# Kernel tuning notes

Hardware: AMD Instinct MI355X
Metric: run time of the kernel (lower is better)

## Reference

```python
import jax, jax.numpy as jnp
import numpy as np
from jax.scipy.stats import norm as jnorm

BLOCK_SIZE = 64
NUM_BITS = 4
OFFSET = 0.9677083


def make_symmetric_nf_table(num_bits=NUM_BITS, offset=OFFSET):
    # create_normal_map(symmetric=True): midpoints of ppf grid, normalized by max
    variations = 2 ** num_bits
    p = jnp.linspace(1.0 - offset, offset, variations + 1)
    v = jnorm.ppf(p)
    vals = 0.5 * (v[:-1] + v[1:])  # [variations]
    vals = jnp.sort(vals)
    return (vals / vals.max()).astype(jnp.float32)


def setup_inputs() -> dict:
    key = jax.random.key(0)
    k1, k2 = jax.random.split(key)
    M, N = 4096, 4096
    T = 8192  # tokens
    x = jax.random.normal(k1, (T, N), dtype=jnp.float32)
    weight = jax.random.normal(k2, (M, N), dtype=jnp.float32) * 0.02
    # init_max_val: per-block abs max of the flattened weight
    wb = weight.reshape(-1, BLOCK_SIZE)
    max_val = jnp.max(jnp.abs(wb), axis=-1)  # [M*N/block_size]
    lookup_table = make_symmetric_nf_table()  # [16]
    return {"x": x, "weight": weight, "max_val": max_val, "lookup_table": lookup_table}


def reference(x, weight, max_val, lookup_table):
    M, N = weight.shape
    # blockwise quantize: [num_blocks, block_size]
    wb = weight.reshape(-1, BLOCK_SIZE)
    wdiv = wb / max_val[:, None]
    # nearest codebook level: [num_blocks, block_size, num_levels] abs-diff argmin
    idx = jnp.argmin(jnp.abs(wdiv[..., None] - lookup_table[None, None, :]), axis=-1)
    qweight = (lookup_table[idx] * max_val[:, None]).reshape(M, N)
    y = x @ qweight.T  # [T, M]
    return (y, qweight)
```

## Files before the change

### kernel.cpp

```cpp
#include <hip/hip_runtime.h>
#include <stdint.h>
#include <stddef.h>

typedef __attribute__((ext_vector_type(8))) short short8;
typedef __attribute__((ext_vector_type(4))) float f32x4;
typedef __attribute__((ext_vector_type(4))) int i32x4;

#define T_DIM 8192
#define M_DIM 4096
#define K_DIM 4096

__device__ __forceinline__ unsigned short f2b(float f) {
    unsigned int u = __builtin_bit_cast(unsigned int, f);
    u += 0x7fffu + ((u >> 16) & 1u);
    return (unsigned short)(u >> 16);
}

__device__ __forceinline__ void async_copy16(const void* g, const void* l) {
    __builtin_amdgcn_global_load_lds(
        (const __attribute__((address_space(1))) unsigned int*)g,
        (__attribute__((address_space(3))) unsigned int*)l,
        16, 0, 0);
}

__global__ __launch_bounds__(512) void prep_all(const float* __restrict__ w,
                                                const float* __restrict__ maxval,
                                                const float* __restrict__ lut_g,
                                                float* __restrict__ qw,
                                                signed char* __restrict__ wq,
                                                float* __restrict__ cw,
                                                const float* __restrict__ x,
                                                signed char* __restrict__ xq,
                                                float* __restrict__ sx) {
    __shared__ float wm[8];
    __shared__ float lut[16];
    const int tid = threadIdx.x;

    if (blockIdx.x < 4096) {
        const int m = blockIdx.x;
        if (tid < 16) lut[tid] = lut_g[tid];

        size_t base = ((size_t)m * 512 + tid) * 8;
        float mv = maxval[base >> 6];

        float mx = mv;
        #pragma unroll
        for (int off = 1; off < 64; off <<= 1)
            mx = fmaxf(mx, __shfl_xor(mx, off, 64));
        if ((tid & 63) == 0) wm[tid >> 6] = mx;
        __syncthreads();
        float cwm = fmaxf(fmaxf(fmaxf(wm[0], wm[1]), fmaxf(wm[2], wm[3])),
                          fmaxf(fmaxf(wm[4], wm[5]), fmaxf(wm[6], wm[7])));

        float4 w0 = *reinterpret_cast<const float4*>(w + base);
        float4 w1 = *reinterpret_cast<const float4*>(w + base + 4);
        float vin[8] = {w0.x, w0.y, w0.z, w0.w, w1.x, w1.y, w1.z, w1.w};
        float outv[8];
        int   li[8];

        #pragma unroll
        for (int e = 0; e < 8; ++e) {
            float v = vin[e] / mv;
            float bd = fabsf(v - lut[0]);
            int best = 0;
            #pragma unroll
            for (int k = 1; k < 16; ++k) {
                float d = fabsf(v - lut[k]);
                if (d < bd) { bd = d; best = k; }
            }
            outv[e] = lut[best] * mv;
            li[e]   = best;
        }

        float4 o0; o0.x = outv[0]; o0.y = outv[1]; o0.z = outv[2]; o0.w = outv[3];
        float4 o1; o1.x = outv[4]; o1.y = outv[5]; o1.z = outv[6]; o1.w = outv[7];
        *reinterpret_cast<float4*>(qw + base)     = o0;
        *reinterpret_cast<float4*>(qw + base + 4) = o1;

        if (wq != nullptr) {
            float s = 127.0f * mv / cwm;
            unsigned u0 = 0, u1 = 0;
            #pragma unroll
            for (int e = 0; e < 4; ++e) {
                int q = (int)rintf(lut[li[e]] * s);
                u0 |= ((unsigned)(q & 255)) << (8 * e);
            }
            #pragma unroll
            for (int e = 0; e < 4; ++e) {
                int q = (int)rintf(lut[li[4 + e]] * s);
                u1 |= ((unsigned)(q & 255)) << (8 * e);
            }
            uint2 pk; pk.x = u0; pk.y = u1;
            *reinterpret_cast<uint2*>(wq + base) = pk;
            if (tid == 0) cw[m] = cwm;
        }
    } else {
        if (xq == nullptr) return;
        const int row = blockIdx.x - 4096;
        const float* xr = x + (size_t)row * K_DIM;

        float4 a = *reinterpret_cast<const float4*>(xr + tid * 8);
        float4 b = *reinterpret_cast<const float4*>(xr + tid * 8 + 4);
        float v[8] = {a.x, a.y, a.z, a.w, b.x, b.y, b.z, b.w};

        float mx = 0.0f;
        #pragma unroll
        for (int e = 0; e < 8; ++e) mx = fmaxf(mx, fabsf(v[e]));
        #pragma unroll
        for (int off = 1; off < 64; off <<= 1)
            mx = fmaxf(mx, __shfl_xor(mx, off, 64));
        if ((tid & 63) == 0) wm[tid >> 6] = mx;
        __syncthreads();
        float rmax = fmaxf(fmaxf(fmaxf(wm[0], wm[1]), fmaxf(wm[2], wm[3])),
                           fmaxf(fmaxf(wm[4], wm[5]), fmaxf(wm[6], wm[7])));
        float inv = rmax > 0.0f ? 127.0f / rmax : 0.0f;

        unsigned u0 = 0, u1 = 0;
        #pragma unroll
        for (int e = 0; e < 4; ++e) {
            int q = (int)rintf(v[e] * inv);
            q = q > 127 ? 127 : (q < -127 ? -127 : q);
            u0 |= ((unsigned)(q & 255)) << (8 * e);
        }
        #pragma unroll
        for (int e = 0; e < 4; ++e) {
            int q = (int)rintf(v[4 + e] * inv);
            q = q > 127 ? 127 : (q < -127 ? -127 : q);
            u1 |= ((unsigned)(q & 255)) << (8 * e);
        }
        uint2 pk; pk.x = u0; pk.y = u1;
        *reinterpret_cast<uint2*>(xq + (size_t)row * K_DIM + tid * 8) = pk;

        if (tid == 0) sx[row] = rmax / 16129.0f;
    }
}


#define RD_A8(BUF, MH)                                                        \
  { _Pragma("unroll") for (int mi = 0; mi < 4; ++mi) {                        \
        int r_ = wr * 64 + mi * 16 + fr;                                      \
        aI[mi] = *reinterpret_cast<const i32x4*>(                             \
            lds + (BUF) * 32768 + (MH) * 16384 + r_ * 64 +                    \
            (fkB ^ (((r_ >> 1) & 3) << 4)));                                  \
  } }

#define RD_B8(BUF, NH, DST)                                                   \
  { _Pragma("unroll") for (int ni = 0; ni < 2; ++ni) {                        \
        int r_ = wc * 32 + ni * 16 + fr;                                      \
        DST[ni] = *reinterpret_cast<const i32x4*>(                            \
            lds + (BUF) * 32768 + ((NH) ? 8192 : 24576) + r_ * 64 +           \
            (fkB ^ (((r_ >> 1) & 3) << 4)));                                  \
  } }

#define MFMA_Q(MH, NH, B)                                                     \
    _Pragma("unroll") for (int mi = 0; mi < 4; ++mi)                          \
    _Pragma("unroll") for (int ni = 0; ni < 2; ++ni)                          \
        acci[(MH) * 4 + mi][(NH) * 2 + ni] =                                  \
            __builtin_amdgcn_mfma_i32_16x16x64_i8(                            \
                aI[mi], B[ni],                                                \
                acci[(MH) * 4 + mi][(NH) * 2 + ni], 0, 0, 0);

#define PH_A(BUF, TNXT)                                                       \
  { RD_A8(BUF, 0)                                                             \
    RD_B8(BUF, 0, bI0)                                                        \
    RD_B8(BUF, 1, bI1)                                                        \
    stage_r2(TNXT);                                                           \
    asm volatile("" ::: "memory");                                            \
    __builtin_amdgcn_s_barrier();                                             \
    asm volatile("" ::: "memory");                                            \
    __builtin_amdgcn_s_setprio(1);                                            \
    MFMA_Q(0, 0, bI0)                                                         \
    MFMA_Q(0, 1, bI1)                                                         \
    __builtin_amdgcn_s_setprio(0); }

#define PH_B(BUF, TNXT2)                                                      \
  { RD_A8(BUF, 1)                                                             \
    stage_r013(TNXT2);                                                        \
    asm volatile("s_waitcnt vmcnt(3)" ::: "memory");                          \
    __builtin_amdgcn_s_barrier();                                             \
    asm volatile("" ::: "memory");                                            \
    __builtin_amdgcn_s_setprio(1);                                            \
    MFMA_Q(1, 1, bI1)                                                         \
    MFMA_Q(1, 0, bI0)                                                         \
    __builtin_amdgcn_s_setprio(0); }

__global__ __launch_bounds__(512, 2) void gemm_i8(
    const signed char* __restrict__ Aq,
    const signed char* __restrict__ Bq,
    const float* __restrict__ sxp,
    const float* __restrict__ cwp,
    float* __restrict__ Y) {
    __shared__ __align__(16) unsigned char lds[65536];

    const int tid  = threadIdx.x;
    const int lane = tid & 63;
    const int wid  = tid >> 6;
    const int wr   = wid >> 2;
    const int wc   = wid & 3;

    const int bid  = blockIdx.x;
    const int swz  = (bid & 7) * 64 + (bid >> 3);
    const int brow = swz >> 4;
    const int bcol = swz & 15;
    const int row0 = brow * 256;
    const int col0 = bcol * 256;

    const int fr  = lane & 15;
    const int fkB = (lane >> 4) * 16;

    i32x4 acci[8][4] = {};
    i32x4 aI[4], bI0[2], bI1[2];

    const int srow  = wid * 16 + (lane >> 2);
    const int sslot = ((lane & 3) ^ ((srow >> 1) & 3)) * 16;
    const unsigned sdst = wid * 1024u;

    auto stage_r013 = [&](int t) {
        int tc  = t < 64 ? t : 63;
        unsigned boff = (unsigned)(t & 1) * 32768u;
        {
            const char* g = (const char*)Aq +
                (size_t)(row0 + ((srow >> 6) << 7) + (srow & 63)) * K_DIM + tc * 64 + sslot;
            async_copy16(g, lds + boff + sdst); }
        {
            const char* g = (const char*)Bq +
                (size_t)(col0 + ((srow >> 5) << 6) + 32 + (srow & 31)) * K_DIM + tc * 64 + sslot;
            async_copy16(g, lds + boff + 8192u + sdst); }
        {
            const char* g = (const char*)Bq +
                (size_t)(col0 + ((srow >> 5) << 6) + (srow & 31)) * K_DIM + tc * 64 + sslot;
            async_copy16(g, lds + boff + 24576u + sdst); }
    };
    auto stage_r2 = [&](int t) {
        int tc  = t < 64 ? t : 63;
        unsigned boff = (unsigned)(t & 1) * 32768u;
        const char* g = (const char*)Aq +
            (size_t)(row0 + 64 + ((srow >> 6) << 7) + (srow & 63)) * K_DIM + tc * 64 + sslot;
        async_copy16(g, lds + boff + 16384u + sdst);
    };

    stage_r013(0);
    stage_r2(0);
    stage_r013(1);
    asm volatile("s_waitcnt vmcnt(3)" ::: "memory");
    __builtin_amdgcn_s_barrier();
    asm volatile("" ::: "memory");

    for (int i = 0; i < 32; ++i) {
        PH_A(0, 2 * i + 1)
        PH_B(0, 2 * i + 2)
        PH_A(1, 2 * i + 2)
        PH_B(1, 2 * i + 3)
    }
    asm volatile("s_waitcnt vmcnt(0)" ::: "memory");

    const int rb = (lane >> 4) * 4;
    float cwv[4];
    #pragma unroll
    for (int n = 0; n < 4; ++n) cwv[n] = cwp[col0 + wc * 64 + n * 16 + fr];
    #pragma unroll
    for (int m = 0; m < 8; ++m) {
        const int t0 = row0 + wr * 128 + m * 16 + rb;
        f32x4 sx4 = *reinterpret_cast<const f32x4*>(sxp + t0);
        #pragma unroll
        for (int n = 0; n < 4; ++n)
            #pragma unroll
            for (int r = 0; r < 4; ++r)
                Y[(size_t)(t0 + r) * M_DIM + col0 + wc * 64 + n * 16 + fr] =
                    (float)acci[m][n][r] * sx4[r] * cwv[n];
    }
}

__global__ __launch_bounds__(256) void gemm_fb(const float* __restrict__ Ap,
                                               const float* __restrict__ Bp,
                                               float* __restrict__ Y) {
    constexpr int BK = 64;
    __shared__ unsigned short lA[128 * BK];
    __shared__ unsigned short lB[128 * BK];

    const int tid  = threadIdx.x;
    const int lane = tid & 63;
    const int wid  = tid >> 6;
    const int wr   = wid >> 1;
    const int wc   = wid & 1;
    const int brow = blockIdx.x >> 5;
    const int bcol = blockIdx.x & 31;
    const int row0 = brow * 128;
    const int col0 = bcol * 128;

    f32x4 acc[4][4] = {};
    const int fr = lane & 15;
    const int fk = (lane >> 4) * 8;
    const int srow = lane >> 3;
    const int scol = (lane & 7) * 8;

    for (int k0 = 0; k0 < K_DIM; k0 += BK) {
        #pragma unroll
        for (int i = 0; i < 4; ++i) {
            const int c = wid * 4 + i;
            const int r = c * 8 + srow;
            const float* g = Ap + (size_t)(row0 + r) * K_DIM + k0 + scol;
            float4 v0 = *reinterpret_cast<const float4*>(g);
            float4 v1 = *reinterpret_cast<const float4*>(g + 4);
            short8 pk;
            pk[0] = (short)f2b(v0.x); pk[1] = (short)f2b(v0.y);
            pk[2] = (short)f2b(v0.z); pk[3] = (short)f2b(v0.w);
            pk[4] = (short)f2b(v1.x); pk[5] = (short)f2b(v1.y);
            pk[6] = (short)f2b(v1.z); pk[7] = (short)f2b(v1.w);
            *reinterpret_cast<short8*>(lA + c * 512 + lane * 8) = pk;
        }
        #pragma unroll
        for (int i = 0; i < 4; ++i) {
            const int c = wid * 4 + i;
            const int r = c * 8 + srow;
            const float* g = Bp + (size_t)(col0 + r) * K_DIM + k0 + scol;
            float4 v0 = *reinterpret_cast<const float4*>(g);
            float4 v1 = *reinterpret_cast<const float4*>(g + 4);
            short8 pk;
            pk[0] = (short)f2b(v0.x); pk[1] = (short)f2b(v0.y);
            pk[2] = (short)f2b(v0.z); pk[3] = (short)f2b(v0.w);
            pk[4] = (short)f2b(v1.x); pk[5] = (short)f2b(v1.y);
            pk[6] = (short)f2b(v1.z); pk[7] = (short)f2b(v1.w);
            *reinterpret_cast<short8*>(lB + c * 512 + lane * 8) = pk;
        }
        __syncthreads();
        #pragma unroll
        for (int kk = 0; kk < BK; kk += 32) {
            short8 af[4], bfr[4];
            #pragma unroll
            for (int m = 0; m < 4; ++m)
                af[m] = *reinterpret_cast<const short8*>(
                    lA + (wr * 64 + m * 16 + fr) * BK + kk + fk);
            #pragma unroll
            for (int n = 0; n < 4; ++n)
                bfr[n] = *reinterpret_cast<const short8*>(
                    lB + (wc * 64 + n * 16 + fr) * BK + kk + fk);
            #pragma unroll
            for (int m = 0; m < 4; ++m)
                #pragma unroll
                for (int n = 0; n < 4; ++n)
                    acc[m][n] = __builtin_amdgcn_mfma_f32_16x16x32_bf16(
                        af[m], bfr[n], acc[m][n], 0, 0, 0);
        }
        __syncthreads();
    }

    const int orow  = row0 + wr * 64;
    const int ocol  = col0 + wc * 64 + fr;
    const int rbase = (lane >> 4) * 4;
    #pragma unroll
    for (int m = 0; m < 4; ++m)
        #pragma unroll
        for (int n = 0; n < 4; ++n)
            #pragma unroll
            for (int r = 0; r < 4; ++r)
                Y[(size_t)(orow + m * 16 + rbase + r) * M_DIM + ocol + n * 16] =
                    acc[m][n][r];
}

extern "C" void kernel_launch(void* const* d_in, const int* in_sizes, int n_in,
                              void* d_out, int out_size, void* d_ws, size_t ws_size,
                              hipStream_t stream) {
    const float* x   = (const float*)d_in[0];
    const float* w   = (const float*)d_in[1];
    const float* mv  = (const float*)d_in[2];
    const float* lut = (const float*)d_in[3];

    float* y  = (float*)d_out;
    float* qw = y + (size_t)T_DIM * M_DIM;

    const bool full = ws_size >= (49u << 20);

    signed char* xq  = (signed char*)d_ws;
    signed char* wqp = xq + (32u << 20);
    float*       sx  = (float*)(xq + (48u << 20));
    float*       cw  = (float*)(xq + (48u << 20) + 65536);

    if (full) {
        prep_all<<<dim3(12288), dim3(512), 0, stream>>>(
            w, mv, lut, qw, wqp, cw, x, xq, sx);
        gemm_i8<<<dim3(512), dim3(512), 0, stream>>>(xq, wqp, sx, cw, y);
    } else {
        prep_all<<<dim3(4096), dim3(512), 0, stream>>>(
            w, mv, lut, qw, nullptr, nullptr, x, nullptr, nullptr);
        dim3 grid((T_DIM / 128) * (M_DIM / 128));
        gemm_fb<<<grid, dim3(256), 0, stream>>>(x, qw, y);
    }
}
```

Baseline: 208.1 us.

## Switch int8 GEMM to triple-buffered LDS with one barrier per k-step

```diff
diff --git a/kernel.cpp b/kernel.cpp
--- a/kernel.cpp
+++ b/kernel.cpp
@@ -136,53 +136,29 @@
 }
 
 
-#define RD_A8(BUF, MH)                                                        \
+#define RD_A8(BOFS, MH, DST)                                                  \
   { _Pragma("unroll") for (int mi = 0; mi < 4; ++mi) {                        \
         int r_ = wr * 64 + mi * 16 + fr;                                      \
-        aI[mi] = *reinterpret_cast<const i32x4*>(                             \
-            lds + (BUF) * 32768 + (MH) * 16384 + r_ * 64 +                    \
+        DST[mi] = *reinterpret_cast<const i32x4*>(                            \
+            lds + (BOFS) + (MH) * 16384 + r_ * 64 +                           \
             (fkB ^ (((r_ >> 1) & 3) << 4)));                                  \
   } }
 
-#define RD_B8(BUF, NH, DST)                                                   \
+#define RD_B8(BOFS, NH, DST)                                                  \
   { _Pragma("unroll") for (int ni = 0; ni < 2; ++ni) {                        \
         int r_ = wc * 32 + ni * 16 + fr;                                      \
         DST[ni] = *reinterpret_cast<const i32x4*>(                            \
-            lds + (BUF) * 32768 + ((NH) ? 8192 : 24576) + r_ * 64 +           \
+            lds + (BOFS) + ((NH) ? 8192 : 24576) + r_ * 64 +                  \
             (fkB ^ (((r_ >> 1) & 3) << 4)));                                  \
   } }
 
-#define MFMA_Q(MH, NH, B)                                                     \
+#define MFMA_Q(MH, NH, A, B)                                                  \
     _Pragma("unroll") for (int mi = 0; mi < 4; ++mi)                          \
     _Pragma("unroll") for (int ni = 0; ni < 2; ++ni)                          \
         acci[(MH) * 4 + mi][(NH) * 2 + ni] =                                  \
             __builtin_amdgcn_mfma_i32_16x16x64_i8(                            \
-                aI[mi], B[ni],                                                \
+                A[mi], B[ni],                                                 \
                 acci[(MH) * 4 + mi][(NH) * 2 + ni], 0, 0, 0);
-
-#define PH_A(BUF, TNXT)                                                       \
-  { RD_A8(BUF, 0)                                                             \
-    RD_B8(BUF, 0, bI0)                                                        \
-    RD_B8(BUF, 1, bI1)                                                        \
-    stage_r2(TNXT);                                                           \
-    asm volatile("" ::: "memory");                                            \
-    __builtin_amdgcn_s_barrier();                                             \
-    asm volatile("" ::: "memory");                                            \
-    __builtin_amdgcn_s_setprio(1);                                            \
-    MFMA_Q(0, 0, bI0)                                                         \
-    MFMA_Q(0, 1, bI1)                                                         \
-    __builtin_amdgcn_s_setprio(0); }
-
-#define PH_B(BUF, TNXT2)                                                      \
-  { RD_A8(BUF, 1)                                                             \
-    stage_r013(TNXT2);                                                        \
-    asm volatile("s_waitcnt vmcnt(3)" ::: "memory");                          \
-    __builtin_amdgcn_s_barrier();                                             \
-    asm volatile("" ::: "memory");                                            \
-    __builtin_amdgcn_s_setprio(1);                                            \
-    MFMA_Q(1, 1, bI1)                                                         \
-    MFMA_Q(1, 0, bI0)                                                         \
-    __builtin_amdgcn_s_setprio(0); }
 
 __global__ __launch_bounds__(512, 2) void gemm_i8(
     const signed char* __restrict__ Aq,
@@ -190,7 +166,7 @@
     const float* __restrict__ sxp,
     const float* __restrict__ cwp,
     float* __restrict__ Y) {
-    __shared__ __align__(16) unsigned char lds[65536];
+    __shared__ __align__(16) unsigned char lds[98304];
 
     const int tid  = threadIdx.x;
     const int lane = tid & 63;
@@ -209,48 +185,56 @@
     const int fkB = (lane >> 4) * 16;
 
     i32x4 acci[8][4] = {};
-    i32x4 aI[4], bI0[2], bI1[2];
+    i32x4 aI0[4], aI1[4], bI0[2], bI1[2];
 
     const int srow  = wid * 16 + (lane >> 2);
     const int sslot = ((lane & 3) ^ ((srow >> 1) & 3)) * 16;
     const unsigned sdst = wid * 1024u;
 
-    auto stage_r013 = [&](int t) {
-        int tc  = t < 64 ? t : 63;
-        unsigned boff = (unsigned)(t & 1) * 32768u;
+    auto stage_all = [&](int t, unsigned bofs) {
+        int tc = t < 64 ? t : 63;
         {
             const char* g = (const char*)Aq +
                 (size_t)(row0 + ((srow >> 6) << 7) + (srow & 63)) * K_DIM + tc * 64 + sslot;
-            async_copy16(g, lds + boff + sdst); }
+            async_copy16(g, lds + bofs + sdst); }
         {
             const char* g = (const char*)Bq +
                 (size_t)(col0 + ((srow >> 5) << 6) + 32 + (srow & 31)) * K_DIM + tc * 64 + sslot;
-            async_copy16(g, lds + boff + 8192u + sdst); }
+            async_copy16(g, lds + bofs + 8192u + sdst); }
+        {
+            const char* g = (const char*)Aq +
+                (size_t)(row0 + 64 + ((srow >> 6) << 7) + (srow & 63)) * K_DIM + tc * 64 + sslot;
+            async_copy16(g, lds + bofs + 16384u + sdst); }
         {
             const char* g = (const char*)Bq +
                 (size_t)(col0 + ((srow >> 5) << 6) + (srow & 31)) * K_DIM + tc * 64 + sslot;
-            async_copy16(g, lds + boff + 24576u + sdst); }
+            async_copy16(g, lds + bofs + 24576u + sdst); }
     };
-    auto stage_r2 = [&](int t) {
-        int tc  = t < 64 ? t : 63;
-        unsigned boff = (unsigned)(t & 1) * 32768u;
-        const char* g = (const char*)Aq +
-            (size_t)(row0 + 64 + ((srow >> 6) << 7) + (srow & 63)) * K_DIM + tc * 64 + sslot;
-        async_copy16(g, lds + boff + 16384u + sdst);
-    };
-
-    stage_r013(0);
-    stage_r2(0);
-    stage_r013(1);
-    asm volatile("s_waitcnt vmcnt(3)" ::: "memory");
+
+    stage_all(0, 0u);
+    stage_all(1, 32768u);
+    asm volatile("s_waitcnt vmcnt(4)" ::: "memory");
     __builtin_amdgcn_s_barrier();
     asm volatile("" ::: "memory");
 
-    for (int i = 0; i < 32; ++i) {
-        PH_A(0, 2 * i + 1)
-        PH_B(0, 2 * i + 2)
-        PH_A(1, 2 * i + 2)
-        PH_B(1, 2 * i + 3)
+    unsigned curo = 0u;
+    for (int t = 0; t < 64; ++t) {
+        unsigned n2o = (curo == 0u) ? 65536u : curo - 32768u;
+        RD_A8(curo, 0, aI0)
+        RD_B8(curo, 0, bI0)
+        RD_B8(curo, 1, bI1)
+        RD_A8(curo, 1, aI1)
+        stage_all(t + 2, n2o);
+        asm volatile("s_waitcnt vmcnt(4)" ::: "memory");
+        __builtin_amdgcn_s_barrier();
+        asm volatile("" ::: "memory");
+        __builtin_amdgcn_s_setprio(1);
+        MFMA_Q(0, 0, aI0, bI0)
+        MFMA_Q(0, 1, aI0, bI1)
+        MFMA_Q(1, 1, aI1, bI1)
+        MFMA_Q(1, 0, aI1, bI0)
+        __builtin_amdgcn_s_setprio(0);
+        curo = (curo == 65536u) ? 0u : curo + 32768u;
     }
     asm volatile("s_waitcnt vmcnt(0)" ::: "memory");
 
```

New measurement: 213.1 us. 1.02x slower.

## Software-pipeline LDS fragment reads one phase ahead of MFMAs

Applied to the files above, without the earlier changes.

```diff
diff --git a/kernel.cpp b/kernel.cpp
--- a/kernel.cpp
+++ b/kernel.cpp
@@ -136,52 +136,52 @@
 }
 
 
-#define RD_A8(BUF, MH)                                                        \
+#define RD_A8(BOFS, MH, DST)                                                  \
   { _Pragma("unroll") for (int mi = 0; mi < 4; ++mi) {                        \
         int r_ = wr * 64 + mi * 16 + fr;                                      \
-        aI[mi] = *reinterpret_cast<const i32x4*>(                             \
-            lds + (BUF) * 32768 + (MH) * 16384 + r_ * 64 +                    \
+        DST[mi] = *reinterpret_cast<const i32x4*>(                            \
+            lds + (BOFS) + (MH) * 16384 + r_ * 64 +                           \
             (fkB ^ (((r_ >> 1) & 3) << 4)));                                  \
   } }
 
-#define RD_B8(BUF, NH, DST)                                                   \
+#define RD_B8(BOFS, NH, DST)                                                  \
   { _Pragma("unroll") for (int ni = 0; ni < 2; ++ni) {                        \
         int r_ = wc * 32 + ni * 16 + fr;                                      \
         DST[ni] = *reinterpret_cast<const i32x4*>(                            \
-            lds + (BUF) * 32768 + ((NH) ? 8192 : 24576) + r_ * 64 +           \
+            lds + (BOFS) + ((NH) ? 8192 : 24576) + r_ * 64 +                  \
             (fkB ^ (((r_ >> 1) & 3) << 4)));                                  \
   } }
 
-#define MFMA_Q(MH, NH, B)                                                     \
+#define MFMA_Q(MH, NH, A, B)                                                  \
     _Pragma("unroll") for (int mi = 0; mi < 4; ++mi)                          \
     _Pragma("unroll") for (int ni = 0; ni < 2; ++ni)                          \
         acci[(MH) * 4 + mi][(NH) * 2 + ni] =                                  \
             __builtin_amdgcn_mfma_i32_16x16x64_i8(                            \
-                aI[mi], B[ni],                                                \
+                A[mi], B[ni],                                                 \
                 acci[(MH) * 4 + mi][(NH) * 2 + ni], 0, 0, 0);
 
-#define PH_A(BUF, TNXT)                                                       \
-  { RD_A8(BUF, 0)                                                             \
-    RD_B8(BUF, 0, bI0)                                                        \
-    RD_B8(BUF, 1, bI1)                                                        \
-    stage_r2(TNXT);                                                           \
+#define PH_A(CBOFS, TNXT, B0C, B1C)                                           \
+  { stage_r2(TNXT);                                                           \
     asm volatile("" ::: "memory");                                            \
     __builtin_amdgcn_s_barrier();                                             \
     asm volatile("" ::: "memory");                                            \
+    RD_A8(CBOFS, 1, aI1)                                                      \
     __builtin_amdgcn_s_setprio(1);                                            \
-    MFMA_Q(0, 0, bI0)                                                         \
-    MFMA_Q(0, 1, bI1)                                                         \
+    MFMA_Q(0, 0, aI0, B0C)                                                    \
+    MFMA_Q(0, 1, aI0, B1C)                                                    \
     __builtin_amdgcn_s_setprio(0); }
 
-#define PH_B(BUF, TNXT2)                                                      \
-  { RD_A8(BUF, 1)                                                             \
-    stage_r013(TNXT2);                                                        \
+#define PH_B(NBOFS, TNXT2, B0C, B1C, B0N, B1N)                                \
+  { stage_r013(TNXT2);                                                        \
     asm volatile("s_waitcnt vmcnt(3)" ::: "memory");                          \
     __builtin_amdgcn_s_barrier();                                             \
     asm volatile("" ::: "memory");                                            \
+    RD_B8(NBOFS, 0, B0N)                                                      \
+    RD_B8(NBOFS, 1, B1N)                                                      \
+    RD_A8(NBOFS, 0, aI0)                                                      \
     __builtin_amdgcn_s_setprio(1);                                            \
-    MFMA_Q(1, 1, bI1)                                                         \
-    MFMA_Q(1, 0, bI0)                                                         \
+    MFMA_Q(1, 1, aI1, B1C)                                                    \
+    MFMA_Q(1, 0, aI1, B0C)                                                    \
     __builtin_amdgcn_s_setprio(0); }
 
 __global__ __launch_bounds__(512, 2) void gemm_i8(
@@ -209,7 +209,8 @@
     const int fkB = (lane >> 4) * 16;
 
     i32x4 acci[8][4] = {};
-    i32x4 aI[4], bI0[2], bI1[2];
+    i32x4 aI0[4], aI1[4];
+    i32x4 bI0a[2], bI1a[2], bI0b[2], bI1b[2];
 
     const int srow  = wid * 16 + (lane >> 2);
     const int sslot = ((lane & 3) ^ ((srow >> 1) & 3)) * 16;
@@ -245,12 +246,15 @@
     asm volatile("s_waitcnt vmcnt(3)" ::: "memory");
     __builtin_amdgcn_s_barrier();
     asm volatile("" ::: "memory");
+    RD_B8(0u, 0, bI0a)
+    RD_B8(0u, 1, bI1a)
+    RD_A8(0u, 0, aI0)
 
     for (int i = 0; i < 32; ++i) {
-        PH_A(0, 2 * i + 1)
-        PH_B(0, 2 * i + 2)
-        PH_A(1, 2 * i + 2)
-        PH_B(1, 2 * i + 3)
+        PH_A(0u,      2 * i + 1, bI0a, bI1a)
+        PH_B(32768u,  2 * i + 2, bI0a, bI1a, bI0b, bI1b)
+        PH_A(32768u,  2 * i + 2, bI0b, bI1b)
+        PH_B(0u,      2 * i + 3, bI0b, bI1b, bI0a, bI1a)
     }
     asm volatile("s_waitcnt vmcnt(0)" ::: "memory");
 
```

Measured after the change: 209.4 us. No clear change (+0.6%).
